# Kernel optimization log

Hardware: AMD Instinct MI355X
Metric: run time of the kernel (lower is better)

## Reference

```python
import jax, jax.numpy as jnp
import numpy as np

D_MODEL = 768
N_HEAD = 12
D_FF = 2048
KEEP_RATIO = 0.6
EPS = 1e-6


def rmsnorm(x, g):
    var = jnp.mean(x * x, axis=-1, keepdims=True)
    return x * jax.lax.rsqrt(var + EPS) * g


def setup_inputs() -> dict:
    key = jax.random.key(0)
    ks = jax.random.split(key, 16)
    B, S, D, F = 2, 2048, D_MODEL, D_FF
    s = 0.02
    inp = {
        "hidden": jax.random.normal(ks[0], (B, S, D), jnp.float32),
        "attn_mask": jnp.tril(jnp.ones((S, S), dtype=bool)),
        "temperature": 1,
        "wq": jax.random.normal(ks[1], (D, D), jnp.float32) * s,
        "wk": jax.random.normal(ks[2], (D, D), jnp.float32) * s,
        "wv": jax.random.normal(ks[3], (D, D), jnp.float32) * s,
        "wo": jax.random.normal(ks[4], (D, D), jnp.float32) * s,
        "w1": jax.random.normal(ks[5], (D, F), jnp.float32) * s,
        "w3": jax.random.normal(ks[6], (D, F), jnp.float32) * s,
        "w2": jax.random.normal(ks[7], (F, D), jnp.float32) * s,
        "g1": jnp.ones((D,), jnp.float32),
        "g2": jnp.ones((D,), jnp.float32),
        "w_mod": jax.random.normal(ks[8], (D,), jnp.float32) * s,
        "b_mod": jnp.zeros((), jnp.float32),
        "w_tok": jax.random.normal(ks[9], (D,), jnp.float32) * s,
        "b_tok": jnp.zeros((), jnp.float32),
        "w_gate": jax.random.normal(ks[10], (D, D), jnp.float32) * s,
        "b_gate": jnp.zeros((D,), jnp.float32),
    }
    return inp


def reference(hidden, attn_mask, temperature, wq, wk, wv, wo, w1, w3, w2,
              g1, g2, w_mod, b_mod, w_tok, b_tok, w_gate, b_gate):
    B, S, D = hidden.shape
    H = N_HEAD
    Dh = D // H

    # depth router: sigmoid(linear / temperature)
    depth_logits = jnp.einsum("bsd,d->bs", hidden, w_mod) + b_mod
    depth_probs = jax.nn.sigmoid(depth_logits / temperature)
    active = (depth_probs > 0.5).astype(hidden.dtype)[..., None]  # [B,S,1]

    normed = rmsnorm(hidden, g1)

    # token router: sigmoid scores, hard top-k keep mask at base keep ratio
    token_scores = jax.nn.sigmoid(jnp.einsum("bsd,d->bs", normed, w_tok) + b_tok)
    k = max(1, int(S * KEEP_RATIO))
    kth = jax.lax.top_k(token_scores, k)[0][:, -1:]  # [B,1]
    token_mask = (token_scores >= kth).astype(hidden.dtype)  # [B,S]

    # multi-head attention over normed
    q = jnp.einsum("bsd,de->bse", normed, wq).reshape(B, S, H, Dh)
    kk = jnp.einsum("bsd,de->bse", normed, wk).reshape(B, S, H, Dh)
    v = jnp.einsum("bsd,de->bse", normed, wv).reshape(B, S, H, Dh)
    logits = jnp.einsum("bqhd,bkhd->bhqk", q, kk) / jnp.sqrt(jnp.float32(Dh))
    logits = jnp.where(attn_mask[None, None, :, :], logits, jnp.float32(-1e9))
    probs = jax.nn.softmax(logits, axis=-1)
    ctx = jnp.einsum("bhqk,bkhd->bqhd", probs, v).reshape(B, S, D)
    attn_out = jnp.einsum("bsd,de->bse", ctx, wo)

    attn_out = attn_out * token_mask[..., None]
    hidden = hidden + attn_out * active  # dropout = identity (eval)

    # ACM gate: x * sigmoid(Wx + b)
    n2 = rmsnorm(hidden, g2)
    gated = n2 * jax.nn.sigmoid(jnp.einsum("bsd,de->bse", n2, w_gate) + b_gate)

    # SwiGLU MLP
    mlp = jnp.einsum("bsf,fd->bsd",
                     jax.nn.silu(jnp.einsum("bsd,df->bsf", gated, w1))
                     * jnp.einsum("bsd,df->bsf", gated, w3), w2)
    hidden = hidden + mlp * active
    return hidden, depth_probs, token_mask
```

## Files before the change

### kernel.cpp

```cpp
#include <hip/hip_runtime.h>


typedef float f32x4 __attribute__((ext_vector_type(4)));
typedef __bf16 bf16x8 __attribute__((ext_vector_type(8)));
typedef __bf16 bf16x4 __attribute__((ext_vector_type(4)));
typedef unsigned int u32;

#define DEV static __device__ __forceinline__

constexpr int SEQ = 2048, DIM = 768, NH = 12;
constexpr int KKEEP = 1228;
constexpr float SCALE2 = 0.125f * 1.4426950408889634f;

DEV f32x4 mfma16(bf16x8 a, bf16x8 b, f32x4 c) {
  return __builtin_amdgcn_mfma_f32_16x16x32_bf16(a, b, c, 0, 0, 0);
}
DEV float sigm(float x) { return 1.0f / (1.0f + __expf(-x)); }
DEV bf16x8 ld8(const __bf16* p) { return *reinterpret_cast<const bf16x8*>(p); }
DEV void st8(__bf16* p, bf16x8 v) { *reinterpret_cast<bf16x8*>(p) = v; }
DEV int swzo(int row, int u) { return row * 64 + ((u ^ (row & 7)) << 3); }

struct Ptr8 { const float* s[8]; };

__global__ void k_transpose_all(Ptr8 pp, __bf16* __restrict__ WT) {
  __shared__ float tile[32][33];
  const int t = blockIdx.x;
  const float* __restrict__ src;
  __bf16* __restrict__ dst;
  int K, N, bx, by, ilv = 0, zofs = 0;
  if (t < 2880) {
    const int mat = t / 576, r = t % 576;
    src = pp.s[mat]; K = 768; N = 768; bx = r % 24; by = r / 24;
    dst = WT + (size_t)mat * 589824;
  } else if (t < 5952) {
    const int tt = t - 2880, mat = tt / 1536, r = tt % 1536;
    src = pp.s[5 + mat]; K = 768; N = 2048; bx = r % 64; by = r / 64;
    dst = WT + 2949120; ilv = 1; zofs = mat * 16;
  } else {
    const int tt = t - 5952;
    src = pp.s[7]; K = 2048; N = 768; bx = tt % 24; by = tt / 24;
    dst = WT + 6094848;
  }
  const int tx = threadIdx.x, ty = threadIdx.y;
  const int n0 = bx * 32, k0 = by * 32;
  for (int i = 0; i < 4; ++i)
    tile[ty + 8 * i][tx] = src[(size_t)(k0 + ty + 8 * i) * N + n0 + tx];
  __syncthreads();
  if (ilv) {
    for (int i = 0; i < 4; ++i) {
      const int n = n0 + ty + 8 * i;
      const int row = ((n >> 4) << 5) + (n & 15) + zofs;
      dst[(size_t)row * K + k0 + tx] = (__bf16)tile[tx][ty + 8 * i];
    }
  } else {
    for (int i = 0; i < 4; ++i)
      dst[(size_t)(n0 + ty + 8 * i) * K + k0 + tx] = (__bf16)tile[tx][ty + 8 * i];
  }
}

__global__ __launch_bounds__(256) void k_router(
    const float* __restrict__ hid, const float* __restrict__ g1,
    const float* __restrict__ wmod, const float* __restrict__ bmod,
    const float* __restrict__ wtok, const float* __restrict__ btok,
    const int* __restrict__ temp, __bf16* __restrict__ normed,
    float* __restrict__ depth_out, float* __restrict__ actF,
    float* __restrict__ tokL) {
  const int t = blockIdx.x, tid = threadIdx.x;
  const float* x = hid + (size_t)t * DIM;
  float xs[3], gs[3], ss = 0.f, dm = 0.f, dt = 0.f;
  for (int j = 0; j < 3; ++j) {
    const int i = tid + 256 * j;
    const float xv = x[i], g = g1[i];
    xs[j] = xv; gs[j] = g;
    ss += xv * xv;
    dm += xv * wmod[i];
    dt += xv * g * wtok[i];
  }
  for (int m = 32; m >= 1; m >>= 1) {
    ss += __shfl_xor(ss, m);
    dm += __shfl_xor(dm, m);
    dt += __shfl_xor(dt, m);
  }
  __shared__ float red[4][3];
  if ((tid & 63) == 0) { red[tid >> 6][0] = ss; red[tid >> 6][1] = dm; red[tid >> 6][2] = dt; }
  __syncthreads();
  ss = red[0][0] + red[1][0] + red[2][0] + red[3][0];
  dm = red[0][1] + red[1][1] + red[2][1] + red[3][1];
  dt = red[0][2] + red[1][2] + red[2][2] + red[3][2];
  const float rms = rsqrtf(ss / 768.0f + 1e-6f);
  if (tid == 0) {
    const int iv = temp[0];
    const float T = (iv > -100000 && iv < 100000) ? (float)iv : __int_as_float(iv);
    const float z = (dm + bmod[0]) / T;
    depth_out[t] = sigm(z);
    actF[t] = z > 0.0f ? 1.0f : 0.0f;
    tokL[t] = rms * dt + btok[0];
  }
  for (int j = 0; j < 3; ++j) {
    const int i = tid + 256 * j;
    normed[(size_t)t * DIM + i] = (__bf16)(xs[j] * rms * gs[j]);
  }
}

__global__ __launch_bounds__(256) void k_count(
    const float* __restrict__ tokL, float* __restrict__ kth_out) {
  const int b = blockIdx.y, tid = threadIdx.x;
  __shared__ float vals[2048];
  const float* L = tokL + (size_t)b * 2048;
#pragma unroll
  for (int j = 0; j < 8; ++j) vals[tid + 256 * j] = L[tid + 256 * j];
  __syncthreads();
  const int cand = blockIdx.x * 128 + (tid >> 1);
  const int half = tid & 1;
  const float e = vals[cand];
  int gt = 0, ge = 0;
  const float4* v4 = reinterpret_cast<const float4*>(vals) + half * 256;
#pragma unroll 8
  for (int j = 0; j < 256; ++j) {
    const float4 q = v4[j];
    gt += (q.x > e) + (q.y > e) + (q.z > e) + (q.w > e);
    ge += (q.x >= e) + (q.y >= e) + (q.z >= e) + (q.w >= e);
  }
  gt += __shfl_xor(gt, 1);
  ge += __shfl_xor(ge, 1);
  if (half == 0 && gt < KKEEP && KKEEP <= ge) kth_out[b] = e;
}

__global__ __launch_bounds__(256) void k_mask(
    const float* __restrict__ tokL, const float* __restrict__ kth,
    const float* __restrict__ actF, float* __restrict__ mask_out,
    float* __restrict__ maskact) {
  const int i = blockIdx.x * 256 + threadIdx.x;
  const int b = i >> 11;
  const float m = (tokL[i] >= kth[b]) ? 1.f : 0.f;
  mask_out[i] = m;
  maskact[i] = m * actF[i];
}

__global__ __launch_bounds__(256) void k_rmsnorm2(
    const float* __restrict__ h2, const float* __restrict__ g2,
    __bf16* __restrict__ n2) {
  const int t = blockIdx.x, tid = threadIdx.x;
  const float* x = h2 + (size_t)t * DIM;
  float xs[3], ss = 0.f;
  for (int j = 0; j < 3; ++j) { const float v = x[tid + 256 * j]; xs[j] = v; ss += v * v; }
  for (int m = 32; m >= 1; m >>= 1) ss += __shfl_xor(ss, m);
  __shared__ float red[4];
  if ((tid & 63) == 0) red[tid >> 6] = ss;
  __syncthreads();
  ss = red[0] + red[1] + red[2] + red[3];
  const float rms = rsqrtf(ss / 768.0f + 1e-6f);
  for (int j = 0; j < 3; ++j) {
    const int i = tid + 256 * j;
    n2[(size_t)t * DIM + i] = (__bf16)(xs[j] * rms * g2[i]);
  }
}

template <int EPI, int MI, int NI>
__global__ __launch_bounds__(256) void k_gemm(
    const __bf16* __restrict__ A, const __bf16* __restrict__ BT,
    int N, int K, size_t bt_stride, size_t out_stride,
    __bf16* __restrict__ outB, float* __restrict__ outF,
    const float* __restrict__ epF, const __bf16* __restrict__ epB,
    const float* __restrict__ rowsc, const float* __restrict__ bias) {
  constexpr int BM = MI * 32, BN = NI * 32;
  __shared__ __align__(16) __bf16 As[BM * 64];
  __shared__ __align__(16) __bf16 Bs[BN * 64];
  const int tid = threadIdx.x;
  const int lane = tid & 63, w = tid >> 6;
  const int wr = w >> 1, wc = w & 1;
  const int f = lane & 15, e = lane >> 4;
  const int m0 = blockIdx.y * BM, n0 = blockIdx.x * BN;
  const __bf16* Bz = BT + (size_t)blockIdx.z * bt_stride;

  const int rowA = (MI == 4) ? (tid >> 1) : (tid >> 2);
  const int uA0  = (MI == 4) ? ((tid & 1) * 4) : ((tid & 3) * 2);
  const int rowB = (NI == 4) ? (tid >> 1) : (tid >> 2);
  const int uB0  = (NI == 4) ? ((tid & 1) * 4) : ((tid & 3) * 2);
  const __bf16* ApR = A + (size_t)(m0 + rowA) * K;
  const __bf16* BpR = Bz + (size_t)(n0 + rowB) * K;

  bf16x8 ya[MI], yb[NI];
  auto LOADY = [&](int k0) {
#pragma unroll
    for (int j = 0; j < MI; ++j) ya[j] = ld8(ApR + k0 + (uA0 + j) * 8);
#pragma unroll
    for (int j = 0; j < NI; ++j) yb[j] = ld8(BpR + k0 + (uB0 + j) * 8);
  };
  auto STORE = [&]() {
#pragma unroll
    for (int j = 0; j < MI; ++j) st8(&As[swzo(rowA, uA0 + j)], ya[j]);
#pragma unroll
    for (int j = 0; j < NI; ++j) st8(&Bs[swzo(rowB, uB0 + j)], yb[j]);
  };

  f32x4 acc[MI][NI] = {};
  LOADY(0);
  for (int k0 = 0; k0 < K; k0 += 64) {
    __syncthreads();
    STORE();
    if (k0 + 64 < K) LOADY(k0 + 64);
    __syncthreads();
    bf16x8 afl[MI], afh[MI], bfl[NI], bfh[NI];
#pragma unroll
    for (int mi = 0; mi < MI; ++mi) {
      const int row = wr * (MI * 16) + mi * 16 + f;
      afl[mi] = ld8(&As[swzo(row, e)]);
      afh[mi] = ld8(&As[swzo(row, e + 4)]);
    }
#pragma unroll
    for (int ni = 0; ni < NI; ++ni) {
      const int row = wc * (NI * 16) + ni * 16 + f;
      bfl[ni] = ld8(&Bs[swzo(row, e)]);
      bfh[ni] = ld8(&Bs[swzo(row, e + 4)]);
    }
#pragma unroll
    for (int mi = 0; mi < MI; ++mi)
#pragma unroll
      for (int ni = 0; ni < NI; ++ni) {
        acc[mi][ni] = mfma16(afl[mi], bfl[ni], acc[mi][ni]);
        acc[mi][ni] = mfma16(afh[mi], bfh[ni], acc[mi][ni]);
      }
  }
  const size_t oz = (size_t)blockIdx.z * out_stride;
  if constexpr (EPI == 5) {
    __bf16* vt = (__bf16*)outF;
    const bool isv = (blockIdx.z == 2);
    const float qs = (blockIdx.z == 0) ? SCALE2 : 1.0f;
#pragma unroll
    for (int mi = 0; mi < MI; ++mi)
#pragma unroll
      for (int ni = 0; ni < NI; ++ni) {
        const int row0 = m0 + wr * (MI * 16) + mi * 16 + e * 4;
        const int col = n0 + wc * (NI * 16) + ni * 16 + f;
        if (!isv) {
#pragma unroll
          for (int r2 = 0; r2 < 4; ++r2)
            outB[oz + (size_t)(row0 + r2) * N + col] =
                (__bf16)(acc[mi][ni][r2] * qs);
        } else {
          bf16x4 pk;
#pragma unroll
          for (int r2 = 0; r2 < 4; ++r2) pk[r2] = (__bf16)acc[mi][ni][r2];
          *reinterpret_cast<bf16x4*>(&vt[(size_t)col * 4096 + row0]) = pk;
        }
      }
  } else if constexpr (EPI == 7) {
    const int NO = N >> 1;
    const int base = n0 + wc * (NI * 16);
    const int jb = ((base >> 5) << 4) + f;
#pragma unroll
    for (int mi = 0; mi < MI; ++mi)
#pragma unroll
      for (int pi = 0; pi < NI / 2; ++pi)
#pragma unroll
        for (int r2 = 0; r2 < 4; ++r2) {
          const float u = acc[mi][2 * pi][r2];
          const float v = acc[mi][2 * pi + 1][r2];
          const int row = m0 + wr * (MI * 16) + mi * 16 + e * 4 + r2;
          outB[(size_t)row * NO + jb + pi * 16] = (__bf16)(u * sigm(u) * v);
        }
  } else {
#pragma unroll
    for (int mi = 0; mi < MI; ++mi)
#pragma unroll
      for (int ni = 0; ni < NI; ++ni)
#pragma unroll
        for (int r2 = 0; r2 < 4; ++r2) {
          const int row = m0 + wr * (MI * 16) + mi * 16 + e * 4 + r2;
          const int col = n0 + wc * (NI * 16) + ni * 16 + f;
          const size_t idx = (size_t)row * N + col;
          const float c = acc[mi][ni][r2];
          if constexpr (EPI == 0) {
            outB[oz + idx] = (__bf16)c;
          } else if constexpr (EPI == 1) {
            outF[idx] = epF[idx] + c * rowsc[row];
          } else if constexpr (EPI == 2) {
            outB[idx] = (__bf16)((float)epB[idx] * sigm(c + bias[col]));
          }
        }
  }
}

__global__ __launch_bounds__(256) void k_attn(
    const __bf16* __restrict__ qb, const __bf16* __restrict__ kb,
    const __bf16* __restrict__ vT, __bf16* __restrict__ Opart,
    float* __restrict__ ml, __bf16* __restrict__ ctxb) {
  __shared__ __bf16 Ks[64 * 64];
  __shared__ __bf16 Vt[64 * 64];
  __shared__ __bf16 Pl[4][16][72];
  const int tid = threadIdx.x, lane = tid & 63, w = tid >> 6;
  const int f = lane & 15, e = lane >> 4;
  const int flat = (int)blockIdx.x;
  const int xcd = flat & 7, r0_ = flat >> 3;
  const int bh = xcd + 8 * (r0_ / 80);
  const int slot_lin = r0_ % 80;
  const int idx = 79 - slot_lin;
  int g4, rel;
  if (idx < 8)       { g4 = 0; rel = idx; }
  else if (idx < 24) { g4 = 1; rel = idx - 8; }
  else if (idx < 48) { g4 = 2; rel = idx - 24; }
  else               { g4 = 3; rel = idx - 48; }
  const int qt = (g4 << 3) + rel / (g4 + 1);
  const int c  = rel % (g4 + 1);
  const int b = bh / NH, h = bh % NH;
  const int slot = bh * 80 + idx;
  const int q0 = qt * 64;
  const int kt0 = c * 8;
  const int ntile = min(8, qt + 1 - kt0);
  const size_t base = (size_t)b * SEQ * DIM + (size_t)h * 64;

  const int qrow = q0 + w * 16 + f;
  const bf16x8 aq0 = ld8(qb + base + (size_t)qrow * DIM + e * 8);
  const bf16x8 aq1 = ld8(qb + base + (size_t)qrow * DIM + 32 + e * 8);
  float lsum[4] = {0.f, 0.f, 0.f, 0.f};
  f32x4 cacc[4];
  for (int g = 0; g < 4; ++g) cacc[g] = f32x4{0.f, 0.f, 0.f, 0.f};

  const int r1 = tid >> 2, u0 = tid & 3;
  const __bf16* kp = kb + base + (size_t)r1 * DIM;
  const __bf16* vp = vT + (size_t)(h * 64 + r1) * 4096 + b * 2048;

  bf16x8 rk0 = ld8(kp + (size_t)(kt0 * 64) * DIM + u0 * 8);
  bf16x8 rk1 = ld8(kp + (size_t)(kt0 * 64) * DIM + (u0 + 4) * 8);
  bf16x8 rv0 = ld8(vp + kt0 * 64 + u0 * 8);
  bf16x8 rv1 = ld8(vp + kt0 * 64 + (u0 + 4) * 8);

  for (int tt = 0; tt < ntile; ++tt) {
    const int kt = kt0 + tt;
    __syncthreads();
    st8(&Ks[swzo(r1, u0)], rk0);  st8(&Ks[swzo(r1, u0 + 4)], rk1);
    st8(&Vt[swzo(r1, u0)], rv0);  st8(&Vt[swzo(r1, u0 + 4)], rv1);
    if (tt + 1 < ntile) {
      const size_t ko = (size_t)((kt + 1) * 64) * DIM;
      rk0 = ld8(kp + ko + u0 * 8);  rk1 = ld8(kp + ko + (u0 + 4) * 8);
      const int vo = (kt + 1) * 64;
      rv0 = ld8(vp + vo + u0 * 8);  rv1 = ld8(vp + vo + (u0 + 4) * 8);
    }
    __syncthreads();

    f32x4 sacc[4];
#pragma unroll
    for (int g = 0; g < 4; ++g) {
      const int row = g * 16 + f;
      f32x4 z = f32x4{0.f, 0.f, 0.f, 0.f};
      z = mfma16(aq0, ld8(&Ks[swzo(row, e)]), z);
      z = mfma16(aq1, ld8(&Ks[swzo(row, e + 4)]), z);
      sacc[g] = z;
    }
    float p[4][4];
    if (kt == qt) {
      const int qg = q0 + w * 16 + e * 4;
#pragma unroll
      for (int g = 0; g < 4; ++g) {
        const int kg = kt * 64 + g * 16 + f;
#pragma unroll
        for (int r = 0; r < 4; ++r) {
          const float pv = (kg > qg + r) ? 0.f : exp2f(sacc[g][r]);
          p[g][r] = pv;
          lsum[r] += pv;
        }
      }
    } else {
#pragma unroll
      for (int g = 0; g < 4; ++g)
#pragma unroll
        for (int r = 0; r < 4; ++r) {
          const float pv = exp2f(sacc[g][r]);
          p[g][r] = pv;
          lsum[r] += pv;
        }
    }
#pragma unroll
    for (int g = 0; g < 4; ++g)
#pragma unroll
      for (int r = 0; r < 4; ++r) Pl[w][e * 4 + r][g * 16 + f] = (__bf16)p[g][r];
    const bf16x8 ap0 = ld8(&Pl[w][f][e * 8]);
    const bf16x8 ap1 = ld8(&Pl[w][f][32 + e * 8]);
#pragma unroll
    for (int g = 0; g < 4; ++g) {
      const int row = g * 16 + f;
      cacc[g] = mfma16(ap0, ld8(&Vt[swzo(row, e)]), cacc[g]);
      cacc[g] = mfma16(ap1, ld8(&Vt[swzo(row, e + 4)]), cacc[g]);
    }
  }
  for (int m = 1; m < 16; m <<= 1)
#pragma unroll
    for (int r = 0; r < 4; ++r) lsum[r] += __shfl_xor(lsum[r], m);
  if (idx < 8) {
    float rl[4];
#pragma unroll
    for (int r = 0; r < 4; ++r) rl[r] = 1.0f / lsum[r];
#pragma unroll
    for (int g = 0; g < 4; ++g)
#pragma unroll
      for (int r = 0; r < 4; ++r) {
        const int row = q0 + w * 16 + e * 4 + r;
        ctxb[base + (size_t)row * DIM + g * 16 + f] =
            (__bf16)(cacc[g][r] * rl[r]);
      }
  } else {
    if (f == 0) {
#pragma unroll
      for (int r = 0; r < 4; ++r)
        ml[(size_t)slot * 64 + w * 16 + e * 4 + r] = lsum[r];
    }
#pragma unroll
    for (int g = 0; g < 4; ++g)
#pragma unroll
      for (int r = 0; r < 4; ++r) {
        const int row = w * 16 + e * 4 + r;
        Opart[(size_t)slot * 4096 + row * 64 + g * 16 + f] = (__bf16)cacc[g][r];
      }
  }
}

__global__ __launch_bounds__(256) void k_attn_combine(
    const __bf16* __restrict__ Opart, const float* __restrict__ ml,
    __bf16* __restrict__ ctxb) {
  const int qt = blockIdx.x + 8, bh = blockIdx.y;
  const int b = bh / NH, h = bh % NH;
  const int g = qt >> 3;
  const int sb = bh * 80 + 4 * g * (g + 1) + (qt & 7) * (g + 1);
  const int nch = g + 1;
  const int row = threadIdx.x >> 2, dh0 = (threadIdx.x & 3) * 16;

  float ltot = 0.f;
  float acc[16];
#pragma unroll
  for (int j = 0; j < 16; ++j) acc[j] = 0.f;
  for (int cc = 0; cc < nch; ++cc) {
    ltot += ml[(size_t)(sb + cc) * 64 + row];
    const __bf16* op = Opart + (size_t)(sb + cc) * 4096 + row * 64 + dh0;
    const bf16x8 o0 = ld8(op), o1 = ld8(op + 8);
#pragma unroll
    for (int j = 0; j < 8; ++j) {
      acc[j] += (float)o0[j];
      acc[8 + j] += (float)o1[j];
    }
  }
  const float rl = 1.0f / ltot;
  bf16x8 w0, w1;
#pragma unroll
  for (int j = 0; j < 8; ++j) {
    w0[j] = (__bf16)(acc[j] * rl);
    w1[j] = (__bf16)(acc[8 + j] * rl);
  }
  const size_t base = (size_t)b * SEQ * DIM + (size_t)h * 64;
  __bf16* dst = ctxb + base + (size_t)(qt * 64 + row) * DIM + dh0;
  st8(dst, w0);
  st8(dst + 8, w1);
}

extern "C" void kernel_launch(void* const* d_in, const int* in_sizes, int n_in,
                              void* d_out, int out_size, void* d_ws, size_t ws_size,
                              hipStream_t stream) {
  const float* hid   = (const float*)d_in[0];
  const int*   temp  = (const int*)d_in[2];
  const float* wq    = (const float*)d_in[3];
  const float* wk    = (const float*)d_in[4];
  const float* wv    = (const float*)d_in[5];
  const float* wo    = (const float*)d_in[6];
  const float* w1    = (const float*)d_in[7];
  const float* w3    = (const float*)d_in[8];
  const float* w2    = (const float*)d_in[9];
  const float* g1    = (const float*)d_in[10];
  const float* g2    = (const float*)d_in[11];
  const float* wmod  = (const float*)d_in[12];
  const float* bmod  = (const float*)d_in[13];
  const float* wtok  = (const float*)d_in[14];
  const float* btok  = (const float*)d_in[15];
  const float* wgate = (const float*)d_in[16];
  const float* bgate = (const float*)d_in[17];

  char* ws = (char*)d_ws;
  __bf16* WT = (__bf16*)ws;
  const size_t oWQ = 0, oWO = 1769472, oWG = 2359296, oW13 = 2949120,
               oW2 = 6094848;
  __bf16* qbuf   = (__bf16*)(ws + 15335424);
  __bf16* kbuf   = qbuf + 3145728;
  __bf16* vTbuf  = kbuf + 3145728;
  __bf16* normed = (__bf16*)(ws + 34209792);
  __bf16* ctxb   = normed + 3145728;
  __bf16* n2buf  = ctxb + 3145728;
  __bf16* tbuf   = normed;
  float*  h2     = (float*)(ws + 53084160);
  __bf16* gated  = (__bf16*)(ws + 65667072);
  __bf16* Opart  = (__bf16*)(ws + 53084160);
  float*  mlbuf  = (float*)(ws + 68812800);
  float*  tokL   = (float*)(ws + 71958528);
  float*  actF   = tokL + 4096;
  float*  maskact = actF + 4096;
  float*  kthbuf  = maskact + 4096;

  float* dout = (float*)d_out;
  float* out_hidden = dout;
  float* out_depth  = dout + 3145728;
  float* out_mask   = dout + 3145728 + 4096;

  Ptr8 p8;
  p8.s[0] = wq; p8.s[1] = wk; p8.s[2] = wv; p8.s[3] = wo; p8.s[4] = wgate;
  p8.s[5] = w1; p8.s[6] = w3; p8.s[7] = w2;
  k_transpose_all<<<7488, dim3(32, 8), 0, stream>>>(p8, WT);

  k_router<<<4096, 256, 0, stream>>>(hid, g1, wmod, bmod, wtok, btok, temp,
                                     normed, out_depth, actF, tokL);
  k_count<<<dim3(16, 2), 256, 0, stream>>>(tokL, kthbuf);
  k_mask<<<16, 256, 0, stream>>>(tokL, kthbuf, actF, out_mask, maskact);

  k_gemm<5, 4, 4><<<dim3(6, 32, 3), 256, 0, stream>>>(
      normed, WT + oWQ, 768, 768, 589824, 3145728,
      qbuf, (float*)vTbuf, nullptr, nullptr, nullptr, nullptr);

  k_attn<<<1920, 256, 0, stream>>>(qbuf, kbuf, vTbuf, Opart, mlbuf, ctxb);
  k_attn_combine<<<dim3(24, 24), 256, 0, stream>>>(Opart, mlbuf, ctxb);

  k_gemm<1, 2, 2><<<dim3(12, 64, 1), 256, 0, stream>>>(
      ctxb, WT + oWO, 768, 768, 0, 0,
      nullptr, h2, hid, nullptr, maskact, nullptr);

  k_rmsnorm2<<<4096, 256, 0, stream>>>(h2, g2, n2buf);

  k_gemm<2, 2, 2><<<dim3(12, 64, 1), 256, 0, stream>>>(
      n2buf, WT + oWG, 768, 768, 0, 0,
      gated, nullptr, nullptr, n2buf, nullptr, bgate);

  k_gemm<7, 4, 4><<<dim3(32, 32, 1), 256, 0, stream>>>(
      gated, WT + oW13, 4096, 768, 0, 0,
      tbuf, nullptr, nullptr, nullptr, nullptr, nullptr);

  k_gemm<1, 2, 2><<<dim3(12, 64, 1), 256, 0, stream>>>(
      tbuf, WT + oW2, 768, 2048, 0, 0,
      nullptr, out_hidden, h2, nullptr, actF, nullptr);

  (void)in_sizes; (void)n_in; (void)out_size; (void)ws_size;
}
```

Before: 184.6 us.

## Enlarge attention query tile to 128 rows per block with split-K chunks

Each attention block now handles 128 query rows (two 16-row fragments per wave) instead of 64, so every K/V tile staged in shared memory is reused by twice as many queries. The chunk scheduling, partial-output slot layout and combine kernel are reworked for 128-row tiles and half as many blocks. This roughly halves global K/V loads per query and the number of partial slots. In exchange it doubles accumulator register use, may reduce occupancy, lowers block count (960) relative to CU count, and adds per-fragment causal branching inside the tile loop.

```diff
diff --git a/kernel.cpp b/kernel.cpp
--- a/kernel.cpp
+++ b/kernel.cpp
@@ -288,34 +288,38 @@
     float* __restrict__ ml, __bf16* __restrict__ ctxb) {
   __shared__ __bf16 Ks[64 * 64];
   __shared__ __bf16 Vt[64 * 64];
-  __shared__ __bf16 Pl[4][16][72];
+  __shared__ __bf16 Pl[4][32][72];
   const int tid = threadIdx.x, lane = tid & 63, w = tid >> 6;
   const int f = lane & 15, e = lane >> 4;
   const int flat = (int)blockIdx.x;
-  const int xcd = flat & 7, r0_ = flat >> 3;
-  const int bh = xcd + 8 * (r0_ / 80);
-  const int slot_lin = r0_ % 80;
-  const int idx = 79 - slot_lin;
-  int g4, rel;
-  if (idx < 8)       { g4 = 0; rel = idx; }
-  else if (idx < 24) { g4 = 1; rel = idx - 8; }
-  else if (idx < 48) { g4 = 2; rel = idx - 24; }
-  else               { g4 = 3; rel = idx - 48; }
-  const int qt = (g4 << 3) + rel / (g4 + 1);
-  const int c  = rel % (g4 + 1);
+  const int xcd = flat & 7, rr = flat >> 3;
+  const int bh = xcd + 8 * (rr / 40);
+  const int slot_lin = rr % 40;
+  const int idx = 39 - slot_lin;
+  int QT, c, nch;
+  if (idx < 4)       { QT = idx;                          c = 0;     nch = 1; }
+  else if (idx < 12) { const int r = idx - 4;  QT = 4 + (r >> 1);  c = r & 1; nch = 2; }
+  else if (idx < 24) { const int r = idx - 12; QT = 8 + r / 3;     c = r % 3; nch = 3; }
+  else               { const int r = idx - 24; QT = 12 + (r >> 2); c = r & 3; nch = 4; }
   const int b = bh / NH, h = bh % NH;
-  const int slot = bh * 80 + idx;
-  const int q0 = qt * 64;
+  const int slot = bh * 40 + idx;
+  const int q0 = QT * 128;
   const int kt0 = c * 8;
-  const int ntile = min(8, qt + 1 - kt0);
+  const int ntile = min(8, 2 * QT + 2 - kt0);
   const size_t base = (size_t)b * SEQ * DIM + (size_t)h * 64;
 
-  const int qrow = q0 + w * 16 + f;
-  const bf16x8 aq0 = ld8(qb + base + (size_t)qrow * DIM + e * 8);
-  const bf16x8 aq1 = ld8(qb + base + (size_t)qrow * DIM + 32 + e * 8);
-  float lsum[4] = {0.f, 0.f, 0.f, 0.f};
-  f32x4 cacc[4];
-  for (int g = 0; g < 4; ++g) cacc[g] = f32x4{0.f, 0.f, 0.f, 0.f};
+  bf16x8 aq[2][2];
+#pragma unroll
+  for (int fi = 0; fi < 2; ++fi) {
+    const int qrow = q0 + w * 32 + fi * 16 + f;
+    aq[fi][0] = ld8(qb + base + (size_t)qrow * DIM + e * 8);
+    aq[fi][1] = ld8(qb + base + (size_t)qrow * DIM + 32 + e * 8);
+  }
+  float lsum[2][4] = {};
+  f32x4 cacc[2][4];
+#pragma unroll
+  for (int fi = 0; fi < 2; ++fi)
+    for (int g = 0; g < 4; ++g) cacc[fi][g] = f32x4{0.f, 0.f, 0.f, 0.f};
 
   const int r1 = tid >> 2, u0 = tid & 3;
   const __bf16* kp = kb + base + (size_t)r1 * DIM;
@@ -339,90 +343,106 @@
     }
     __syncthreads();
 
-    f32x4 sacc[4];
-#pragma unroll
-    for (int g = 0; g < 4; ++g) {
-      const int row = g * 16 + f;
-      f32x4 z = f32x4{0.f, 0.f, 0.f, 0.f};
-      z = mfma16(aq0, ld8(&Ks[swzo(row, e)]), z);
-      z = mfma16(aq1, ld8(&Ks[swzo(row, e + 4)]), z);
-      sacc[g] = z;
-    }
-    float p[4][4];
-    if (kt == qt) {
-      const int qg = q0 + w * 16 + e * 4;
+#pragma unroll
+    for (int fi = 0; fi < 2; ++fi) {
+      const int qtf = (q0 + w * 32 + fi * 16) >> 6;
+      if (kt > qtf) continue;
+      f32x4 sacc[4];
 #pragma unroll
       for (int g = 0; g < 4; ++g) {
-        const int kg = kt * 64 + g * 16 + f;
+        const int row = g * 16 + f;
+        f32x4 z = f32x4{0.f, 0.f, 0.f, 0.f};
+        z = mfma16(aq[fi][0], ld8(&Ks[swzo(row, e)]), z);
+        z = mfma16(aq[fi][1], ld8(&Ks[swzo(row, e + 4)]), z);
+        sacc[g] = z;
+      }
+      float p[4][4];
+      if (kt == qtf) {
+        const int qg = q0 + w * 32 + fi * 16 + e * 4;
+#pragma unroll
+        for (int g = 0; g < 4; ++g) {
+          const int kg = kt * 64 + g * 16 + f;
+#pragma unroll
+          for (int r = 0; r < 4; ++r) {
+            const float pv = (kg > qg + r) ? 0.f : exp2f(sacc[g][r]);
+            p[g][r] = pv;
+            lsum[fi][r] += pv;
+          }
+        }
+      } else {
+#pragma unroll
+        for (int g = 0; g < 4; ++g)
+#pragma unroll
+          for (int r = 0; r < 4; ++r) {
+            const float pv = exp2f(sacc[g][r]);
+            p[g][r] = pv;
+            lsum[fi][r] += pv;
+          }
+      }
+#pragma unroll
+      for (int g = 0; g < 4; ++g)
+#pragma unroll
+        for (int r = 0; r < 4; ++r)
+          Pl[w][fi * 16 + e * 4 + r][g * 16 + f] = (__bf16)p[g][r];
+      const bf16x8 ap0 = ld8(&Pl[w][fi * 16 + f][e * 8]);
+      const bf16x8 ap1 = ld8(&Pl[w][fi * 16 + f][32 + e * 8]);
+#pragma unroll
+      for (int g = 0; g < 4; ++g) {
+        const int row = g * 16 + f;
+        cacc[fi][g] = mfma16(ap0, ld8(&Vt[swzo(row, e)]), cacc[fi][g]);
+        cacc[fi][g] = mfma16(ap1, ld8(&Vt[swzo(row, e + 4)]), cacc[fi][g]);
+      }
+    }
+  }
+  for (int m = 1; m < 16; m <<= 1)
+#pragma unroll
+    for (int fi = 0; fi < 2; ++fi)
+#pragma unroll
+      for (int r = 0; r < 4; ++r) lsum[fi][r] += __shfl_xor(lsum[fi][r], m);
+  if (nch == 1) {
+#pragma unroll
+    for (int fi = 0; fi < 2; ++fi) {
+      float rl[4];
+#pragma unroll
+      for (int r = 0; r < 4; ++r) rl[r] = 1.0f / lsum[fi][r];
+#pragma unroll
+      for (int g = 0; g < 4; ++g)
 #pragma unroll
         for (int r = 0; r < 4; ++r) {
-          const float pv = (kg > qg + r) ? 0.f : exp2f(sacc[g][r]);
-          p[g][r] = pv;
-          lsum[r] += pv;
+          const int row = q0 + w * 32 + fi * 16 + e * 4 + r;
+          ctxb[base + (size_t)row * DIM + g * 16 + f] =
+              (__bf16)(cacc[fi][g][r] * rl[r]);
         }
-      }
-    } else {
-#pragma unroll
-      for (int g = 0; g < 4; ++g)
-#pragma unroll
-        for (int r = 0; r < 4; ++r) {
-          const float pv = exp2f(sacc[g][r]);
-          p[g][r] = pv;
-          lsum[r] += pv;
-        }
-    }
-#pragma unroll
-    for (int g = 0; g < 4; ++g)
-#pragma unroll
-      for (int r = 0; r < 4; ++r) Pl[w][e * 4 + r][g * 16 + f] = (__bf16)p[g][r];
-    const bf16x8 ap0 = ld8(&Pl[w][f][e * 8]);
-    const bf16x8 ap1 = ld8(&Pl[w][f][32 + e * 8]);
-#pragma unroll
-    for (int g = 0; g < 4; ++g) {
-      const int row = g * 16 + f;
-      cacc[g] = mfma16(ap0, ld8(&Vt[swzo(row, e)]), cacc[g]);
-      cacc[g] = mfma16(ap1, ld8(&Vt[swzo(row, e + 4)]), cacc[g]);
-    }
-  }
-  for (int m = 1; m < 16; m <<= 1)
-#pragma unroll
-    for (int r = 0; r < 4; ++r) lsum[r] += __shfl_xor(lsum[r], m);
-  if (idx < 8) {
-    float rl[4];
-#pragma unroll
-    for (int r = 0; r < 4; ++r) rl[r] = 1.0f / lsum[r];
-#pragma unroll
-    for (int g = 0; g < 4; ++g)
-#pragma unroll
-      for (int r = 0; r < 4; ++r) {
-        const int row = q0 + w * 16 + e * 4 + r;
-        ctxb[base + (size_t)row * DIM + g * 16 + f] =
-            (__bf16)(cacc[g][r] * rl[r]);
-      }
+    }
   } else {
     if (f == 0) {
 #pragma unroll
-      for (int r = 0; r < 4; ++r)
-        ml[(size_t)slot * 64 + w * 16 + e * 4 + r] = lsum[r];
-    }
-#pragma unroll
-    for (int g = 0; g < 4; ++g)
-#pragma unroll
-      for (int r = 0; r < 4; ++r) {
-        const int row = w * 16 + e * 4 + r;
-        Opart[(size_t)slot * 4096 + row * 64 + g * 16 + f] = (__bf16)cacc[g][r];
-      }
-  }
-}
-
-__global__ __launch_bounds__(256) void k_attn_combine(
+      for (int fi = 0; fi < 2; ++fi)
+#pragma unroll
+        for (int r = 0; r < 4; ++r)
+          ml[(size_t)slot * 128 + w * 32 + fi * 16 + e * 4 + r] = lsum[fi][r];
+    }
+#pragma unroll
+    for (int fi = 0; fi < 2; ++fi)
+#pragma unroll
+      for (int g = 0; g < 4; ++g)
+#pragma unroll
+        for (int r = 0; r < 4; ++r) {
+          const int row = w * 32 + fi * 16 + e * 4 + r;
+          Opart[(size_t)slot * 8192 + row * 64 + g * 16 + f] =
+              (__bf16)cacc[fi][g][r];
+        }
+  }
+}
+
+__global__ __launch_bounds__(512) void k_attn_combine(
     const __bf16* __restrict__ Opart, const float* __restrict__ ml,
     __bf16* __restrict__ ctxb) {
-  const int qt = blockIdx.x + 8, bh = blockIdx.y;
+  const int QT = blockIdx.x + 4, bh = blockIdx.y;
   const int b = bh / NH, h = bh % NH;
-  const int g = qt >> 3;
-  const int sb = bh * 80 + 4 * g * (g + 1) + (qt & 7) * (g + 1);
-  const int nch = g + 1;
+  const int g2 = QT >> 2;
+  const int sb = bh * 40 + 2 * g2 * (g2 + 1) + (QT & 3) * (g2 + 1);
+  const int nch = g2 + 1;
   const int row = threadIdx.x >> 2, dh0 = (threadIdx.x & 3) * 16;
 
   float ltot = 0.f;
@@ -430,8 +450,8 @@
 #pragma unroll
   for (int j = 0; j < 16; ++j) acc[j] = 0.f;
   for (int cc = 0; cc < nch; ++cc) {
-    ltot += ml[(size_t)(sb + cc) * 64 + row];
-    const __bf16* op = Opart + (size_t)(sb + cc) * 4096 + row * 64 + dh0;
+    ltot += ml[(size_t)(sb + cc) * 128 + row];
+    const __bf16* op = Opart + (size_t)(sb + cc) * 8192 + row * 64 + dh0;
     const bf16x8 o0 = ld8(op), o1 = ld8(op + 8);
 #pragma unroll
     for (int j = 0; j < 8; ++j) {
@@ -447,7 +467,7 @@
     w1[j] = (__bf16)(acc[8 + j] * rl);
   }
   const size_t base = (size_t)b * SEQ * DIM + (size_t)h * 64;
-  __bf16* dst = ctxb + base + (size_t)(qt * 64 + row) * DIM + dh0;
+  __bf16* dst = ctxb + base + (size_t)(QT * 128 + row) * DIM + dh0;
   st8(dst, w0);
   st8(dst + 8, w1);
 }
@@ -512,8 +532,8 @@
       normed, WT + oWQ, 768, 768, 589824, 3145728,
       qbuf, (float*)vTbuf, nullptr, nullptr, nullptr, nullptr);
 
-  k_attn<<<1920, 256, 0, stream>>>(qbuf, kbuf, vTbuf, Opart, mlbuf, ctxb);
-  k_attn_combine<<<dim3(24, 24), 256, 0, stream>>>(Opart, mlbuf, ctxb);
+  k_attn<<<960, 256, 0, stream>>>(qbuf, kbuf, vTbuf, Opart, mlbuf, ctxb);
+  k_attn_combine<<<dim3(12, 24), 512, 0, stream>>>(Opart, mlbuf, ctxb);
 
   k_gemm<1, 2, 2><<<dim3(12, 64, 1), 256, 0, stream>>>(
       ctxb, WT + oWO, 768, 768, 0, 0,
```

New measurement: 191.4 us. 3.7% more time.
